# Optimization experiments

Hardware: AMD Instinct MI355X
Metric: run time of the kernel (lower is better)

Reference implementation:

```python
import jax, jax.numpy as jnp
import numpy as np

N_HEADS = 16
KV_HEADS = 4
D_HEAD = 64
D_MODEL = 1024
NUM_BUCKETS = 32
MAX_DISTANCE = 128


def _relative_position_bucket(relative_position, num_buckets=NUM_BUCKETS, max_distance=MAX_DISTANCE):
    # Bidirectional (encoder) T5 bucket function.
    nb = num_buckets // 2
    rel_buckets = (relative_position > 0).astype(jnp.int32) * nb
    rp = jnp.abs(relative_position)
    max_exact = nb // 2
    is_small = rp < max_exact
    rp_safe = jnp.maximum(rp, 1).astype(jnp.float32)
    rp_large = max_exact + (
        jnp.log(rp_safe / max_exact) / np.log(max_distance / max_exact) * (nb - max_exact)
    ).astype(jnp.int32)
    rp_large = jnp.minimum(rp_large, nb - 1)
    return rel_buckets + jnp.where(is_small, rp, rp_large)


def compute_bias(rel_bias, q_len, k_len):
    context_pos = jnp.arange(q_len)[:, None]
    memory_pos = jnp.arange(k_len)[None, :]
    buckets = _relative_position_bucket(memory_pos - context_pos)  # [q, k]
    values = rel_bias[buckets]                                     # [q, k, H]
    return jnp.transpose(values, (2, 0, 1))[None]                  # [1, H, q, k]


def setup_inputs() -> dict:
    key = jax.random.key(0)
    ks = jax.random.split(key, 6)
    scale = D_MODEL ** -0.5
    return {
        "hidden_states": jax.random.normal(ks[0], (4, 2048, D_MODEL), jnp.float32),
        "Wq": jax.random.normal(ks[1], (N_HEADS * D_HEAD, D_MODEL), jnp.float32) * scale,
        "Wk": jax.random.normal(ks[2], (N_HEADS * D_HEAD, D_MODEL), jnp.float32) * scale,
        "Wv": jax.random.normal(ks[3], (N_HEADS * D_HEAD, D_MODEL), jnp.float32) * scale,
        "Wo": jax.random.normal(ks[4], (D_MODEL, N_HEADS * D_HEAD), jnp.float32) * scale,
        "rel_bias": jax.random.normal(ks[5], (NUM_BUCKETS, N_HEADS), jnp.float32),
    }


def reference(hidden_states, Wq, Wk, Wv, Wo, rel_bias):
    B, N, _ = hidden_states.shape
    G = N_HEADS // KV_HEADS
    # projections: torch Linear -> x @ W.T; shape to [b, heads, n, d]
    q = (hidden_states @ Wq.T).reshape(B, N, N_HEADS, D_HEAD).transpose(0, 2, 1, 3)
    k = (hidden_states @ Wk.T).reshape(B, N, N_HEADS, D_HEAD).transpose(0, 2, 1, 3)
    v = (hidden_states @ Wv.T).reshape(B, N, N_HEADS, D_HEAD).transpose(0, 2, 1, 3)
    # split heads into (g, h) groups with h = kv_heads as inner index
    gq = q.reshape(B, G, KV_HEADS, N, D_HEAD)
    gk = k.reshape(B, G, KV_HEADS, N, D_HEAD).mean(axis=1)  # [b, h, n, d]
    gv = v.reshape(B, G, KV_HEADS, N, D_HEAD).mean(axis=1)
    # NOTE: einsum sums queries over the group axis g (faithful to source)
    scores = jnp.einsum('bghnd,bhsd->bhns', gq, gk)
    bias = compute_bias(rel_bias, N, N)                      # [1, H, n, n]
    gbias = bias.reshape(1, G, KV_HEADS, N, N).mean(axis=1)  # [1, h, n, n]
    scores = scores + gbias
    attn = jax.nn.softmax(scores.astype(jnp.float32), axis=-1).astype(scores.dtype)
    out = jnp.einsum('bhns,bhsd->bhnd', attn, gv)
    out = out.transpose(0, 2, 1, 3).reshape(B, N, KV_HEADS * D_HEAD)
    out = jnp.tile(out, (1, 1, G))  # repeat 'b s d -> b s (g d)'
    return out @ Wo.T
```

## Files before the change

kernel.cpp:

```cpp
#include <hip/hip_runtime.h>
#include <math.h>

typedef _Float16 half_t;
typedef _Float16 half4 __attribute__((ext_vector_type(4)));
typedef _Float16 half8 __attribute__((ext_vector_type(8)));
typedef float f32x4 __attribute__((ext_vector_type(4)));

#define LOG2E 1.44269504088896f

__device__ __forceinline__ void gload16(const void* g, void* l) {
    __builtin_amdgcn_global_load_lds(
        (const __attribute__((address_space(1))) unsigned int*)g,
        (__attribute__((address_space(3))) unsigned int*)l, 16, 0, 0);
}

__global__ __launch_bounds__(256) void prep(const float* __restrict__ hs,
                     const float* __restrict__ Wq, const float* __restrict__ Wk,
                     const float* __restrict__ Wv, const float* __restrict__ Wo,
                     const float* __restrict__ rb,
                     half_t* __restrict__ hsh,
                     half_t* __restrict__ Wqkv, half_t* __restrict__ Wo_e,
                     float* __restrict__ btab) {
    if (blockIdx.x < 4096) {
        int i = (blockIdx.x * 256 + threadIdx.x) * 8;
        f32x4 a = *(const f32x4*)&hs[i];
        f32x4 b = *(const f32x4*)&hs[i + 4];
        half8 o;
        #pragma unroll
        for (int j = 0; j < 4; ++j) { o[j] = (half_t)a[j]; o[4 + j] = (half_t)b[j]; }
        *(half8*)&hsh[i] = o;
        return;
    }
    int idx = (blockIdx.x - 4096) * 256 + threadIdx.x;
    if (idx < 768 * 1024) {
        int row = idx >> 10, col = idx & 1023;
        int sec = row >> 8;
        int r = row & 255;
        int h = r >> 6, d = r & 63;
        const float* W = (sec == 0) ? Wq : ((sec == 1) ? Wk : Wv);
        float s = 0.f;
        #pragma unroll
        for (int g = 0; g < 4; ++g) s += W[((g * 4 + h) * 64 + d) * 1024 + col];
        s *= (sec == 0) ? LOG2E : 0.25f;
        Wqkv[idx] = (half_t)s;
    }
    if (idx < 1024 * 256) {
        int m = idx >> 8, c = idx & 255;
        float s = 0.f;
        #pragma unroll
        for (int g = 0; g < 4; ++g) s += Wo[m * 1024 + g * 256 + c];
        Wo_e[idx] = (half_t)s;
    }
    if (idx < 4 * 4096) {
        int h = idx >> 12, dpos = idx & 4095;
        int delta = dpos - 2048;
        int bucket = (delta > 0) ? 16 : 0;
        int ad = delta < 0 ? -delta : delta;
        if (ad < 8) bucket += ad;
        else {
            int large = 8 + (int)(logf((float)ad * 0.125f) / logf(16.0f) * 8.0f);
            bucket += (large < 15) ? large : 15;
        }
        float s = 0.f;
        #pragma unroll
        for (int g = 0; g < 4; ++g) s += rb[bucket * 16 + g * 4 + h];
        btab[idx] = s * 0.25f * LOG2E;
    }
}

__global__ __launch_bounds__(256) void gemm_nt_mfma(const half_t* __restrict__ A,
                                                    const half_t* __restrict__ B,
                                                    void* __restrict__ Cptr,
                                                    int M, int N, int K, int store_half,
                                                    half_t* __restrict__ vtp) {
    __shared__ __attribute__((aligned(16))) half_t As[128 * 64];
    __shared__ __attribute__((aligned(16))) half_t Bs[64 * 64];
    int tid = threadIdx.x;
    int w = tid >> 6, lane = tid & 63;
    int c = lane & 15, quad = lane >> 4;
    int rowBase = blockIdx.y * 128, colBase = blockIdx.x * 64;
    int wr = (w & 1) * 64, wc = (w >> 1) * 32;

    f32x4 acc[4][2];
    #pragma unroll
    for (int i = 0; i < 4; ++i)
        #pragma unroll
        for (int j = 0; j < 2; ++j) acc[i][j] = (f32x4)(0.f);

    int srow = tid >> 3;
    int kcs = ((tid & 7) ^ (srow & 7)) * 8;
    int rx = c & 7;

    for (int k0 = 0; k0 < K; k0 += 64) {
        __syncthreads();
        #pragma unroll
        for (int p = 0; p < 4; ++p)
            gload16(&A[(size_t)(rowBase + srow + 32 * p) * K + k0 + kcs],
                    &As[p * 2048 + w * 512]);
        #pragma unroll
        for (int p = 0; p < 2; ++p)
            gload16(&B[(size_t)(colBase + srow + 32 * p) * K + k0 + kcs],
                    &Bs[p * 2048 + w * 512]);
        __syncthreads();

        #pragma unroll
        for (int kh = 0; kh < 2; ++kh) {
            int xk = ((quad + 4 * kh) ^ rx) * 8;
            half8 af[4], bf[2];
            #pragma unroll
            for (int i = 0; i < 4; ++i)
                af[i] = *(const half8*)&As[(wr + i * 16 + c) * 64 + xk];
            #pragma unroll
            for (int j = 0; j < 2; ++j)
                bf[j] = *(const half8*)&Bs[(wc + j * 16 + c) * 64 + xk];
            #pragma unroll
            for (int i = 0; i < 4; ++i)
                #pragma unroll
                for (int j = 0; j < 2; ++j)
                    acc[i][j] = __builtin_amdgcn_mfma_f32_16x16x32_f16(af[i], bf[j], acc[i][j], 0, 0, 0);
        }
    }

    if (vtp && colBase >= 512) {
        int h = (colBase - 512) >> 6;
        #pragma unroll
        for (int i = 0; i < 4; ++i)
            #pragma unroll
            for (int j = 0; j < 2; ++j) {
                int row0 = rowBase + wr + i * 16 + quad * 4;
                int dd = wc + j * 16 + c;
                int b = row0 >> 11, n = row0 & 2047;
                half4 pk;
                #pragma unroll
                for (int reg = 0; reg < 4; ++reg) pk[reg] = (half_t)acc[i][j][reg];
                *(half4*)&vtp[((size_t)((b * 4 + h) * 64 + dd)) * 2048 + n] = pk;
            }
        return;
    }

    #pragma unroll
    for (int i = 0; i < 4; ++i)
        #pragma unroll
        for (int j = 0; j < 2; ++j)
            #pragma unroll
            for (int reg = 0; reg < 4; ++reg) {
                size_t row = rowBase + wr + i * 16 + quad * 4 + reg;
                size_t col = colBase + wc + j * 16 + c;
                if (store_half) ((half_t*)Cptr)[row * N + col] = (half_t)acc[i][j][reg];
                else            ((float*)Cptr)[row * N + col] = acc[i][j][reg];
            }
}

__global__ __launch_bounds__(256) void attn(const half_t* __restrict__ qkv,
                                            const half_t* __restrict__ vt,
                                            const float* __restrict__ btab,
                                            half_t* __restrict__ Opart,
                                            float* __restrict__ ml) {
    __shared__ __attribute__((aligned(16))) half_t Ks[2][64 * 64];
    __shared__ __attribute__((aligned(16))) half_t Vts[2][64 * 64];
    __shared__ __attribute__((aligned(16))) half_t Ps[4 * 16 * 64];

    int tid = threadIdx.x;
    int w = tid >> 6, lane = tid & 63;
    int c = lane & 15, quad = lane >> 4;
    int qt = blockIdx.x, h = blockIdx.y;
    int b = blockIdx.z >> 1, s = blockIdx.z & 1;
    int q0 = qt * 64;
    int bh = b * 4 + h;
    int k0g = s * 1024;

    const half_t* qrow = qkv + (size_t)(b * 2048 + q0 + w * 16 + c) * 768 + h * 64;
    half8 qf0 = *(const half8*)(qrow + quad * 8);
    half8 qf1 = *(const half8*)(qrow + 32 + quad * 8);

    float cpos = btab[h * 4096 + 4095];
    float cneg = btab[h * 4096];

    const float* bpt = btab + h * 4096 + 2048 + k0g - (q0 + w * 16 + c);

    int srow = tid >> 3;
    int kcs = ((tid & 7) ^ (srow & 7)) * 8;
    const half_t* gK = qkv + (size_t)(b * 2048 + k0g + srow) * 768 + 256 + h * 64 + kcs;
    const half_t* gV = vt + (size_t)(bh * 64 + srow) * 2048 + k0g + kcs;

    auto stage = [&](int it2) {
        int bb = it2 & 1;
        const half_t* gKt = gK + (size_t)(it2 * 64) * 768;
        const half_t* gVt = gV + it2 * 64;
        gload16(gKt,                     &Ks[bb][w * 512]);
        gload16(gKt + (size_t)32 * 768,  &Ks[bb][2048 + w * 512]);
        gload16(gVt,                     &Vts[bb][w * 512]);
        gload16(gVt + 32 * 2048,         &Vts[bb][2048 + w * 512]);
    };

    f32x4 O[4];
    #pragma unroll
    for (int i = 0; i < 4; ++i) O[i] = (f32x4)(0.f);
    float mrow = -1e30f, lrow = 0.f;

    int rx = c & 7;
    half_t* pw = &Ps[w * 16 * 64];

    stage(0);
    __syncthreads();

    for (int it = 0; it < 16; ++it) {
        int ktg = k0g + it * 64;
        if (it < 15) stage(it + 1);
        const half_t* Kb = Ks[it & 1];
        const half_t* Vb = Vts[it & 1];

        f32x4 ST[4];
        __builtin_amdgcn_s_setprio(1);
        #pragma unroll
        for (int kb = 0; kb < 4; ++kb) {
            int row = kb * 16 + c;
            half8 kf0 = *(const half8*)&Kb[row * 64 + (quad ^ rx) * 8];
            half8 kf1 = *(const half8*)&Kb[row * 64 + ((quad + 4) ^ rx) * 8];
            f32x4 a = (f32x4)(0.f);
            a = __builtin_amdgcn_mfma_f32_16x16x32_f16(kf0, qf0, a, 0, 0, 0);
            a = __builtin_amdgcn_mfma_f32_16x16x32_f16(kf1, qf1, a, 0, 0, 0);
            ST[kb] = a;
        }
        __builtin_amdgcn_s_setprio(0);

        float cb;
        if (ktg >= q0 + 191) {
            cb = cpos;
        } else if (ktg + 191 <= q0) {
            cb = cneg;
        } else {
            cb = 0.f;
            const float* bp = bpt + it * 64;
            #pragma unroll
            for (int kb = 0; kb < 4; ++kb)
                #pragma unroll
                for (int rg = 0; rg < 4; ++rg)
                    ST[kb][rg] += bp[kb * 16 + quad * 4 + rg];
        }

        float tmax = -1e30f;
        #pragma unroll
        for (int kb = 0; kb < 4; ++kb)
            #pragma unroll
            for (int rg = 0; rg < 4; ++rg) tmax = fmaxf(tmax, ST[kb][rg]);
        tmax += cb;
        tmax = fmaxf(tmax, __shfl_xor(tmax, 16));
        tmax = fmaxf(tmax, __shfl_xor(tmax, 32));

        float mnew = fmaxf(mrow, tmax);
        float alpha = exp2f(mrow - mnew);
        mrow = mnew;
        float madj = mnew - cb;

        float lsum = 0.f;
        #pragma unroll
        for (int kb = 0; kb < 4; ++kb) {
            half4 pk;
            #pragma unroll
            for (int rg = 0; rg < 4; ++rg) {
                float p = exp2f(ST[kb][rg] - madj);
                lsum += p;
                pk[rg] = (half_t)p;
            }
            *(half4*)&pw[c * 64 + ((4 * kb + quad + 2 * c) & 15) * 4] = pk;
        }
        lrow = lrow * alpha + lsum;
        __asm__ __volatile__("s_waitcnt lgkmcnt(0)" ::: "memory");

        half8 pf0 = *(const half8*)&pw[c * 64 + ((2 * quad + 2 * c) & 15) * 4];
        half8 pf1 = *(const half8*)&pw[c * 64 + ((8 + 2 * quad + 2 * c) & 15) * 4];
        __builtin_amdgcn_s_setprio(1);
        #pragma unroll
        for (int db = 0; db < 4; ++db) {
            int row = db * 16 + c;
            half8 vf0 = *(const half8*)&Vb[row * 64 + (quad ^ rx) * 8];
            half8 vf1 = *(const half8*)&Vb[row * 64 + ((quad + 4) ^ rx) * 8];
            f32x4 o = O[db];
            #pragma unroll
            for (int rg = 0; rg < 4; ++rg) o[rg] *= alpha;
            o = __builtin_amdgcn_mfma_f32_16x16x32_f16(vf0, pf0, o, 0, 0, 0);
            o = __builtin_amdgcn_mfma_f32_16x16x32_f16(vf1, pf1, o, 0, 0, 0);
            O[db] = o;
        }
        __builtin_amdgcn_s_setprio(0);

        __asm__ __volatile__("s_waitcnt vmcnt(0)" ::: "memory");
        __builtin_amdgcn_s_barrier();
    }

    lrow += __shfl_xor(lrow, 16);
    lrow += __shfl_xor(lrow, 32);
    float inv = 1.0f / lrow;

    int pb = (bh * 32 + qt) * 2 + s;
    #pragma unroll
    for (int db = 0; db < 4; ++db) {
        half4 pk;
        #pragma unroll
        for (int rg = 0; rg < 4; ++rg) pk[rg] = (half_t)(O[db][rg] * inv);
        *(half4*)&Opart[((size_t)pb * 64 + w * 16 + c) * 64 + db * 16 + quad * 4] = pk;
    }
    if (quad == 0) {
        ml[pb * 128 + w * 16 + c] = mrow;
        ml[pb * 128 + 64 + w * 16 + c] = lrow;
    }
}

__global__ __launch_bounds__(256) void merge(const half_t* __restrict__ Opart,
                                             const float* __restrict__ ml,
                                             half_t* __restrict__ ab) {
    int bq = blockIdx.x;
    int bh = bq >> 5, qt = bq & 31;
    int b = bh >> 2, h = bh & 3;
    int row = threadIdx.x >> 2;
    int cg = (threadIdx.x & 3) * 16;
    int p0 = bq * 2, p1 = p0 + 1;
    float m1 = ml[p0 * 128 + row], l1 = ml[p0 * 128 + 64 + row];
    float m2 = ml[p1 * 128 + row], l2 = ml[p1 * 128 + 64 + row];
    float m = fmaxf(m1, m2);
    float a1 = exp2f(m1 - m) * l1, a2 = exp2f(m2 - m) * l2;
    float inv = 1.f / (a1 + a2);
    float w1 = a1 * inv, w2 = a2 * inv;
    const half8* o1 = (const half8*)&Opart[((size_t)p0 * 64 + row) * 64 + cg];
    const half8* o2 = (const half8*)&Opart[((size_t)p1 * 64 + row) * 64 + cg];
    half_t* dst = ab + (size_t)(b * 2048 + qt * 64 + row) * 256 + h * 64 + cg;
    #pragma unroll
    for (int v = 0; v < 2; ++v) {
        half8 x = o1[v], y = o2[v], o;
        #pragma unroll
        for (int j = 0; j < 8; ++j)
            o[j] = (half_t)((float)x[j] * w1 + (float)y[j] * w2);
        *(half8*)(dst + v * 8) = o;
    }
}

extern "C" void kernel_launch(void* const* d_in, const int* in_sizes, int n_in,
                              void* d_out, int out_size, void* d_ws, size_t ws_size,
                              hipStream_t stream) {
    (void)in_sizes; (void)n_in; (void)out_size; (void)ws_size;
    const float* hs = (const float*)d_in[0];
    const float* Wq = (const float*)d_in[1];
    const float* Wk = (const float*)d_in[2];
    const float* Wv = (const float*)d_in[3];
    const float* Wo = (const float*)d_in[4];
    const float* rb = (const float*)d_in[5];

    char* p = (char*)d_ws;
    half_t* Wqkv = (half_t*)p;            p += 768 * 1024 * 2;
    half_t* Wo_e = (half_t*)p;            p += 1024 * 256 * 2;
    float*  btab = (float*)p;             p += 4 * 4096 * 4;
    char*   hshp = p;                     p += (size_t)8192 * 1024 * 2;
    half_t* qkv  = (half_t*)p;            p += (size_t)8192 * 768 * 2;
    half_t* vt   = (half_t*)p;            p += (size_t)16 * 64 * 2048 * 2;
    half_t* hsh   = (half_t*)hshp;
    half_t* Opart = (half_t*)hshp;
    float*  mlbuf = (float*)(hshp + (size_t)1024 * 64 * 64 * 2);
    half_t* ab    = (half_t*)(hshp + (size_t)9 * 1024 * 1024);
    float*  out  = (float*)d_out;

    prep<<<7168, 256, 0, stream>>>(hs, Wq, Wk, Wv, Wo, rb, hsh, Wqkv, Wo_e, btab);

    gemm_nt_mfma<<<dim3(12, 64), 256, 0, stream>>>(hsh, Wqkv, qkv, 8192, 768, 1024, 1, vt);

    attn<<<dim3(32, 4, 8), 256, 0, stream>>>(qkv, vt, btab, Opart, mlbuf);
    merge<<<512, 256, 0, stream>>>(Opart, mlbuf, ab);

    gemm_nt_mfma<<<dim3(16, 64), 256, 0, stream>>>(ab, Wo_e, out, 8192, 1024, 256, 0, nullptr);
}
```

Baseline: 177.4 us.

## Double-buffer GEMM with 128x128 tiles and remap block order for locality

The GEMM kernel now uses 128x128 output tiles with double-buffered LDS staging. It prefetches the next K slice while computing the current one, raises wave priority during the MFMA section, and uses a single barrier per step. Grids for the GEMMs and attention are flattened and reordered so consecutive blocks share the same weight or KV tiles, which should improve cache reuse. Doubling LDS and accumulators cuts occupancy, and the projection GEMM now launches fewer blocks (384), which may underfill the GPU.

```diff
diff --git a/kernel.cpp b/kernel.cpp
--- a/kernel.cpp
+++ b/kernel.cpp
@@ -71,69 +71,83 @@
 __global__ __launch_bounds__(256) void gemm_nt_mfma(const half_t* __restrict__ A,
                                                     const half_t* __restrict__ B,
                                                     void* __restrict__ Cptr,
-                                                    int M, int N, int K, int store_half,
+                                                    int N, int K, int store_half,
                                                     half_t* __restrict__ vtp) {
-    __shared__ __attribute__((aligned(16))) half_t As[128 * 64];
-    __shared__ __attribute__((aligned(16))) half_t Bs[64 * 64];
+    __shared__ __attribute__((aligned(16))) half_t As[2][128 * 64];
+    __shared__ __attribute__((aligned(16))) half_t Bs[2][128 * 64];
     int tid = threadIdx.x;
     int w = tid >> 6, lane = tid & 63;
     int c = lane & 15, quad = lane >> 4;
-    int rowBase = blockIdx.y * 128, colBase = blockIdx.x * 64;
-    int wr = (w & 1) * 64, wc = (w >> 1) * 32;
-
-    f32x4 acc[4][2];
+    int flat = blockIdx.x;
+    int rowBase = (flat & 63) * 128;
+    int colBase = (flat >> 6) * 128;
+    int wr = (w & 1) * 64, wc = (w >> 1) * 64;
+
+    f32x4 acc[4][4];
     #pragma unroll
     for (int i = 0; i < 4; ++i)
         #pragma unroll
-        for (int j = 0; j < 2; ++j) acc[i][j] = (f32x4)(0.f);
+        for (int j = 0; j < 4; ++j) acc[i][j] = (f32x4)(0.f);
 
     int srow = tid >> 3;
     int kcs = ((tid & 7) ^ (srow & 7)) * 8;
     int rx = c & 7;
-
-    for (int k0 = 0; k0 < K; k0 += 64) {
-        __syncthreads();
+    int nsteps = K >> 6;
+
+    auto stage = [&](int ks) {
+        int bb = ks & 1;
         #pragma unroll
         for (int p = 0; p < 4; ++p)
-            gload16(&A[(size_t)(rowBase + srow + 32 * p) * K + k0 + kcs],
-                    &As[p * 2048 + w * 512]);
-        #pragma unroll
-        for (int p = 0; p < 2; ++p)
-            gload16(&B[(size_t)(colBase + srow + 32 * p) * K + k0 + kcs],
-                    &Bs[p * 2048 + w * 512]);
-        __syncthreads();
-
+            gload16(&A[(size_t)(rowBase + srow + 32 * p) * K + ks * 64 + kcs],
+                    &As[bb][p * 2048 + w * 512]);
+        #pragma unroll
+        for (int p = 0; p < 4; ++p)
+            gload16(&B[(size_t)(colBase + srow + 32 * p) * K + ks * 64 + kcs],
+                    &Bs[bb][p * 2048 + w * 512]);
+    };
+
+    stage(0);
+    __syncthreads();
+
+    for (int ks = 0; ks < nsteps; ++ks) {
+        if (ks + 1 < nsteps) stage(ks + 1);
+        const half_t* Ab = As[ks & 1];
+        const half_t* Bb = Bs[ks & 1];
+        __builtin_amdgcn_s_setprio(1);
         #pragma unroll
         for (int kh = 0; kh < 2; ++kh) {
             int xk = ((quad + 4 * kh) ^ rx) * 8;
-            half8 af[4], bf[2];
+            half8 af[4], bf[4];
             #pragma unroll
             for (int i = 0; i < 4; ++i)
-                af[i] = *(const half8*)&As[(wr + i * 16 + c) * 64 + xk];
-            #pragma unroll
-            for (int j = 0; j < 2; ++j)
-                bf[j] = *(const half8*)&Bs[(wc + j * 16 + c) * 64 + xk];
+                af[i] = *(const half8*)&Ab[(wr + i * 16 + c) * 64 + xk];
+            #pragma unroll
+            for (int j = 0; j < 4; ++j)
+                bf[j] = *(const half8*)&Bb[(wc + j * 16 + c) * 64 + xk];
             #pragma unroll
             for (int i = 0; i < 4; ++i)
                 #pragma unroll
-                for (int j = 0; j < 2; ++j)
+                for (int j = 0; j < 4; ++j)
                     acc[i][j] = __builtin_amdgcn_mfma_f32_16x16x32_f16(af[i], bf[j], acc[i][j], 0, 0, 0);
         }
+        __builtin_amdgcn_s_setprio(0);
+        __asm__ __volatile__("s_waitcnt vmcnt(0)" ::: "memory");
+        __builtin_amdgcn_s_barrier();
     }
 
     if (vtp && colBase >= 512) {
-        int h = (colBase - 512) >> 6;
         #pragma unroll
         for (int i = 0; i < 4; ++i)
             #pragma unroll
-            for (int j = 0; j < 2; ++j) {
+            for (int j = 0; j < 4; ++j) {
                 int row0 = rowBase + wr + i * 16 + quad * 4;
-                int dd = wc + j * 16 + c;
+                int vcol = colBase - 512 + wc + j * 16 + c;
+                int hh = vcol >> 6, dd = vcol & 63;
                 int b = row0 >> 11, n = row0 & 2047;
                 half4 pk;
                 #pragma unroll
                 for (int reg = 0; reg < 4; ++reg) pk[reg] = (half_t)acc[i][j][reg];
-                *(half4*)&vtp[((size_t)((b * 4 + h) * 64 + dd)) * 2048 + n] = pk;
+                *(half4*)&vtp[((size_t)((b * 4 + hh) * 64 + dd)) * 2048 + n] = pk;
             }
         return;
     }
@@ -141,7 +155,7 @@
     #pragma unroll
     for (int i = 0; i < 4; ++i)
         #pragma unroll
-        for (int j = 0; j < 2; ++j)
+        for (int j = 0; j < 4; ++j)
             #pragma unroll
             for (int reg = 0; reg < 4; ++reg) {
                 size_t row = rowBase + wr + i * 16 + quad * 4 + reg;
@@ -163,8 +177,12 @@
     int tid = threadIdx.x;
     int w = tid >> 6, lane = tid & 63;
     int c = lane & 15, quad = lane >> 4;
-    int qt = blockIdx.x, h = blockIdx.y;
-    int b = blockIdx.z >> 1, s = blockIdx.z & 1;
+    int flat = blockIdx.x;
+    int g = flat & 31;
+    int qt = flat >> 5;
+    int h = g & 3;
+    int zz = g >> 2;
+    int b = zz >> 1, s = zz & 1;
     int q0 = qt * 64;
     int bh = b * 4 + h;
     int k0g = s * 1024;
@@ -361,10 +379,10 @@
 
     prep<<<7168, 256, 0, stream>>>(hs, Wq, Wk, Wv, Wo, rb, hsh, Wqkv, Wo_e, btab);
 
-    gemm_nt_mfma<<<dim3(12, 64), 256, 0, stream>>>(hsh, Wqkv, qkv, 8192, 768, 1024, 1, vt);
-
-    attn<<<dim3(32, 4, 8), 256, 0, stream>>>(qkv, vt, btab, Opart, mlbuf);
+    gemm_nt_mfma<<<6 * 64, 256, 0, stream>>>(hsh, Wqkv, qkv, 768, 1024, 1, vt);
+
+    attn<<<1024, 256, 0, stream>>>(qkv, vt, btab, Opart, mlbuf);
     merge<<<512, 256, 0, stream>>>(Opart, mlbuf, ab);
 
-    gemm_nt_mfma<<<dim3(16, 64), 256, 0, stream>>>(ab, Wo_e, out, 8192, 1024, 256, 0, nullptr);
-}
+    gemm_nt_mfma<<<8 * 64, 256, 0, stream>>>(ab, Wo_e, out, 1024, 256, 0, nullptr);
+}
```

After: 175.4 us. Within noise of the previous version (-1.1%).
